# Kernel optimization log

Hardware: AMD Instinct MI355X
Metric: run time of the kernel (lower is better)

Reference implementation:

```python
import jax, jax.numpy as jnp
import numpy as np

B, HORIZON, F, ORDER, K = 8192, 64, 64, 16, 256


def setup_inputs() -> dict:
    key = jax.random.key(0)
    ks = jax.random.split(key, 7)
    s = 0.05
    x = jax.random.normal(ks[0], (B, HORIZON, F), dtype=jnp.float32)
    y0 = jax.random.normal(ks[1], (B, ORDER), dtype=jnp.float32)
    kernel = jax.random.normal(ks[2], (F + ORDER, 4 * K), dtype=jnp.float32) * s
    rec_kernel = jax.random.normal(ks[3], (K, 4 * K), dtype=jnp.float32) * s
    bias = jax.random.normal(ks[4], (4 * K,), dtype=jnp.float32) * s
    dense_w = jax.random.normal(ks[5], (K, 1), dtype=jnp.float32) * s
    dense_b = jax.random.normal(ks[6], (1,), dtype=jnp.float32) * s
    return {"x": x, "y0": y0, "kernel": kernel, "rec_kernel": rec_kernel,
            "bias": bias, "dense_w": dense_w, "dense_b": dense_b}


def reference(x, y0, kernel, rec_kernel, bias, dense_w, dense_b):
    Bn = x.shape[0]
    Ku = rec_kernel.shape[0]
    h0 = jnp.zeros((Bn, Ku), x.dtype)
    c0 = jnp.zeros((Bn, Ku), x.dtype)

    def step(carry, x_t):
        h, c, yp = carry  # yp: [B, order], newest prediction first
        inp = jnp.concatenate([x_t, yp], axis=1)          # [B, F+order]
        z = inp @ kernel + h @ rec_kernel + bias          # [B, 4K]
        i, f, g, o = jnp.split(z, 4, axis=1)              # Keras gate order i,f,c,o
        i = jax.nn.sigmoid(i)
        f = jax.nn.sigmoid(f)
        g = jnp.tanh(g)
        o = jax.nn.sigmoid(o)
        c_new = f * c + i * g
        h_new = o * jnp.tanh(c_new)
        pred = h_new @ dense_w + dense_b                  # [B, 1]
        # tf.roll(shift=1)[:, 1:] then concat([pred, .]) == shift-in newest pred
        yp_new = jnp.concatenate([pred, yp[:, :-1]], axis=1)
        return (h_new, c_new, yp_new), pred

    xs = jnp.transpose(x, (1, 0, 2))                      # [horizon, B, F]
    _, preds = jax.lax.scan(step, (h0, c0, y0), xs)       # preds: [horizon, B, 1]
    return jnp.transpose(preds, (1, 0, 2))                # [B, horizon, 1]
```

## Files before the change

### kernel.cpp

```cpp
#include <hip/hip_runtime.h>
#include <stdint.h>


typedef short v8s __attribute__((ext_vector_type(8)));
typedef float v4f __attribute__((ext_vector_type(4)));

#define NKS 11
#define NKCOL 1024
#define PKR 1
#define PKL 2
#define SK0 (PKR + PKL)

__device__ __forceinline__ unsigned bf16u(float f) {
  unsigned u = __float_as_uint(f);
  return (u + 0x7FFFu + ((u >> 16) & 1u)) >> 16;
}
__device__ __forceinline__ float sigm(float x) {
  return __builtin_amdgcn_rcpf(1.f + __expf(-x));
}
__device__ __forceinline__ float tanh_(float x) {
  return 1.f - 2.f * __builtin_amdgcn_rcpf(1.f + __expf(2.f * x));
}
__device__ __forceinline__ int a_addr(int m, int k) {
  return (((m >> 4) * NKS + (k >> 5)) << 10)
       + ((((k >> 3) & 3) * 16 + (m & 15)) << 4)
       + ((k & 7) << 1);
}

__global__ void prep_w(const float* __restrict__ ker, const float* __restrict__ rec,
                       uint4* __restrict__ wsw) {
  int tid = blockIdx.x * 256 + threadIdx.x;
  int lane = tid & 63;
  int rest = tid >> 6;
  int ks = rest % NKS;
  int nt = rest / NKS;
  int n  = nt * 16 + (lane & 15);
  int k0 = ks * 32 + ((lane >> 4) & 3) * 8;
  unsigned h[8];
  #pragma unroll
  for (int j = 0; j < 8; ++j) {
    int k = k0 + j;
    float v = 0.f;
    if (k < 80)       v = ker[k * NKCOL + n];
    else if (k < 336) v = rec[(k - 80) * NKCOL + n];
    h[j] = bf16u(v);
  }
  uint4 o;
  o.x = h[0] | (h[1] << 16); o.y = h[2] | (h[3] << 16);
  o.z = h[4] | (h[5] << 16); o.w = h[6] | (h[7] << 16);
  wsw[tid] = o;
}

__global__ __launch_bounds__(512, 2)
void lstm_main(const float* __restrict__ x, const float* __restrict__ y0,
               const float* __restrict__ bias, const float* __restrict__ dw,
               const float* __restrict__ db, const v8s* __restrict__ wv,
               float* __restrict__ out) {
  __shared__ __align__(16) char a_lds[2 * NKS * 1024];
  __shared__ __align__(16) v8s w_lds[PKL * 64 * 64];
  __shared__ float predbuf[32][8];
  __shared__ float predf[32];

  const int tid  = threadIdx.x;
  const int lane = tid & 63;
  const int wave = tid >> 6;
  const int l15  = lane & 15;
  const int quad = lane >> 4;
  const int b0   = blockIdx.x * 32;

  for (int i = tid; i < 2 * NKS * 256; i += 512) ((unsigned*)a_lds)[i] = 0;
  for (int i = tid; i < PKL * 64 * 64; i += 512) {
    int ksl = i >> 12;
    int nt  = (i >> 6) & 63;
    int ln  = i & 63;
    w_lds[i] = wv[(nt * NKS + PKR + ksl) * 64 + ln];
  }

  float bias_v[8];
  int wb[8], wlo[8];
  #pragma unroll
  for (int ln = 0; ln < 8; ++ln) {
    int g = ln >> 1, s = ln & 1;
    int ntg = g * 16 + wave * 2 + s;
    wb[ln]  = ntg * NKS * 64;
    wlo[ln] = ntg * 64 + lane;
    bias_v[ln] = bias[ntg * 16 + l15];
  }
  float dw_v[2];
  dw_v[0] = dw[wave * 32 + l15];
  dw_v[1] = dw[wave * 32 + 16 + l15];
  const float dbv = db[0];

  v8s wreg[8];
  #pragma unroll
  for (int ln = 0; ln < 8; ++ln)
    wreg[ln] = wv[wb[ln] + lane];

  float cst[2][2][4];
  #pragma unroll
  for (int mt = 0; mt < 2; ++mt)
    #pragma unroll
    for (int s = 0; s < 2; ++s)
      #pragma unroll
      for (int r = 0; r < 4; ++r) cst[mt][s][r] = 0.f;

  const int ms_x  = tid >> 3;
  const int kq8_x = tid & 7;
  const int ms_y  = (tid - 256) >> 3;
  const int jj    = tid & 7;
  float4 xpa, xpb;
  if (tid < 256) {
    const float* xp = x + ((size_t)((b0 + ms_x) * 64)) * 64 + kq8_x * 8;
    xpa = ((const float4*)xp)[0];
    xpb = ((const float4*)xp)[1];
  }

  __syncthreads();

  #pragma unroll 1
  for (int t = 0; t < 64; ++t) {
    unsigned xw[4];
    unsigned short q0 = 0, q1 = 0;
    float pin = 0.f;
    if (tid < 256) {
      xw[0] = bf16u(xpa.x) | (bf16u(xpa.y) << 16);
      xw[1] = bf16u(xpa.z) | (bf16u(xpa.w) << 16);
      xw[2] = bf16u(xpb.x) | (bf16u(xpb.y) << 16);
      xw[3] = bf16u(xpb.z) | (bf16u(xpb.w) << 16);
    } else {
      if (t == 0) {
        q0 = (unsigned short)bf16u(y0[(b0 + ms_y) * 16 + 2 * jj]);
        q1 = (unsigned short)bf16u(y0[(b0 + ms_y) * 16 + 2 * jj + 1]);
      } else {
        q0 = *(const unsigned short*)(a_lds + a_addr(ms_y, 64 + 2 * jj));
        q1 = *(const unsigned short*)(a_lds + a_addr(ms_y, 64 + 2 * jj + 1));
        pin = predf[ms_y];
      }
    }
    __syncthreads();
    if (tid < 256) {
      uint4 w4; w4.x = xw[0]; w4.y = xw[1]; w4.z = xw[2]; w4.w = xw[3];
      *(uint4*)(a_lds + a_addr(ms_x, kq8_x * 8)) = w4;
    } else {
      if (t == 0) {
        *(unsigned short*)(a_lds + a_addr(ms_y, 64 + 2 * jj))     = q0;
        *(unsigned short*)(a_lds + a_addr(ms_y, 64 + 2 * jj + 1)) = q1;
      } else {
        if (jj < 7) {
          *(unsigned short*)(a_lds + a_addr(ms_y, 64 + 2 * jj + 1)) = q0;
          *(unsigned short*)(a_lds + a_addr(ms_y, 64 + 2 * jj + 2)) = q1;
        } else {
          *(unsigned short*)(a_lds + a_addr(ms_y, 79)) = q0;
        }
        if (jj == 0)
          *(unsigned short*)(a_lds + a_addr(ms_y, 64)) = (unsigned short)bf16u(pin);
      }
    }
    __syncthreads();

    if (t < 63 && tid < 256) {
      const float* xp = x + ((size_t)((b0 + ms_x) * 64 + (t + 1))) * 64 + kq8_x * 8;
      xpa = ((const float4*)xp)[0];
      xpb = ((const float4*)xp)[1];
    }

    v4f acc[2][8];
    #pragma unroll
    for (int mt = 0; mt < 2; ++mt)
      #pragma unroll
      for (int ln = 0; ln < 8; ++ln) acc[mt][ln] = v4f{0.f, 0.f, 0.f, 0.f};

    v8s bs0[8], bs1[8];
    #pragma unroll
    for (int ln = 0; ln < 8; ++ln) bs0[ln] = wv[wb[ln] + SK0 * 64 + lane];
    v8s af0 = *(const v8s*)(a_lds + (lane << 4));
    v8s af1 = *(const v8s*)(a_lds + (NKS << 10) + (lane << 4));

    #define MFMA_BLK(ksi, W8)                                                   \
      do {                                                                      \
        v8s c0 = af0, c1 = af1;                                                 \
        if ((ksi) < NKS - 1) {                                                  \
          af0 = *(const v8s*)(a_lds + (((ksi) + 1) << 10) + (lane << 4));       \
          af1 = *(const v8s*)(a_lds + ((NKS + (ksi) + 1) << 10) + (lane << 4)); \
        }                                                                       \
        _Pragma("unroll")                                                       \
        for (int ln = 0; ln < 8; ++ln) {                                        \
          acc[0][ln] = __builtin_amdgcn_mfma_f32_16x16x32_bf16(c0, W8[ln], acc[0][ln], 0, 0, 0); \
          acc[1][ln] = __builtin_amdgcn_mfma_f32_16x16x32_bf16(c1, W8[ln], acc[1][ln], 0, 0, 0); \
        }                                                                       \
      } while (0)
    #define REFILL(BUF, rks)                                                    \
      do {                                                                      \
        _Pragma("unroll")                                                       \
        for (int ln = 0; ln < 8; ++ln)                                          \
          BUF[ln] = wv[wb[ln] + (rks) * 64 + lane];                             \
      } while (0)

    MFMA_BLK(0, wreg);

    {
      v8s wl[8];
      #pragma unroll
      for (int ln = 0; ln < 8; ++ln) wl[ln] = w_lds[wlo[ln]];
      REFILL(bs1, SK0 + 1);
      MFMA_BLK(1, wl);
      #pragma unroll
      for (int ln = 0; ln < 8; ++ln) wl[ln] = w_lds[4096 + wlo[ln]];
      MFMA_BLK(2, wl);
    }

    MFMA_BLK(3, bs0);  REFILL(bs0, 5);
    MFMA_BLK(4, bs1);  REFILL(bs1, 6);
    MFMA_BLK(5, bs0);  REFILL(bs0, 7);
    MFMA_BLK(6, bs1);  REFILL(bs1, 8);
    MFMA_BLK(7, bs0);  REFILL(bs0, 9);
    MFMA_BLK(8, bs1);  REFILL(bs1, 10);
    MFMA_BLK(9, bs0);
    MFMA_BLK(10, bs1);

    #undef MFMA_BLK
    #undef REFILL

    __syncthreads();

    float padd[2][4];
    #pragma unroll
    for (int mt = 0; mt < 2; ++mt)
      #pragma unroll
      for (int r = 0; r < 4; ++r) padd[mt][r] = 0.f;

    #pragma unroll
    for (int mt = 0; mt < 2; ++mt) {
      #pragma unroll
      for (int s = 0; s < 2; ++s) {
        const int kk = 80 + wave * 32 + s * 16 + l15;
        #pragma unroll
        for (int r = 0; r < 4; ++r) {
          float zi = acc[mt][0 + s][r] + bias_v[0 + s];
          float zf = acc[mt][2 + s][r] + bias_v[2 + s];
          float zg = acc[mt][4 + s][r] + bias_v[4 + s];
          float zo = acc[mt][6 + s][r] + bias_v[6 + s];
          float is = sigm(zi), fs = sigm(zf), gs = tanh_(zg), os = sigm(zo);
          float cn = fs * cst[mt][s][r] + is * gs;
          cst[mt][s][r] = cn;
          float hh = os * tanh_(cn);
          int m = mt * 16 + quad * 4 + r;
          *(unsigned short*)(a_lds + a_addr(m, kk)) = (unsigned short)bf16u(hh);
          padd[mt][r] += hh * dw_v[s];
        }
      }
    }
    #pragma unroll
    for (int mt = 0; mt < 2; ++mt) {
      #pragma unroll
      for (int r = 0; r < 4; ++r) {
        float p = padd[mt][r];
        p += __shfl_xor(p, 1);
        p += __shfl_xor(p, 2);
        p += __shfl_xor(p, 4);
        p += __shfl_xor(p, 8);
        if (l15 == 0) predbuf[mt * 16 + quad * 4 + r][wave] = p;
      }
    }
    __syncthreads();
    if (tid < 32) {
      float p = dbv;
      #pragma unroll
      for (int w = 0; w < 8; ++w) p += predbuf[tid][w];
      out[(size_t)(b0 + tid) * 64 + t] = p;
      predf[tid] = p;
    }
    __syncthreads();
  }
}

extern "C" void kernel_launch(void* const* d_in, const int* in_sizes, int n_in,
                              void* d_out, int out_size, void* d_ws, size_t ws_size,
                              hipStream_t stream) {
  const float* x    = (const float*)d_in[0];
  const float* y0   = (const float*)d_in[1];
  const float* ker  = (const float*)d_in[2];
  const float* rec  = (const float*)d_in[3];
  const float* bias = (const float*)d_in[4];
  const float* dw   = (const float*)d_in[5];
  const float* db   = (const float*)d_in[6];

  prep_w<<<dim3(176), dim3(256), 0, stream>>>(ker, rec, (uint4*)d_ws);
  lstm_main<<<dim3(256), dim3(512), 0, stream>>>(x, y0, bias, dw, db,
                                                 (const v8s*)d_ws, (float*)d_out);
}
```

Measured before the change: 1.292 ms.

## Reorder weight staging, prefetch global weights across steps, batch output stores

Moves the first two k-slices of weights into LDS instead of one register slice plus two LDS slices. The first two global weight slices are now preloaded before the time loop and refilled at the end of each step, so the loads for the next step overlap the current step's tail. The x prefetch for the next step moves after the MFMA section, and predictions are buffered in LDS and written as float4 every 16 steps instead of as scalar stores every step. This aims to hide global load latency and cut uncoalesced stores, at the cost of holding two weight register buffers for the whole loop, which raises register pressure.

```diff
diff --git a/kernel.cpp b/kernel.cpp
--- a/kernel.cpp
+++ b/kernel.cpp
@@ -7,9 +7,8 @@
 
 #define NKS 11
 #define NKCOL 1024
-#define PKR 1
 #define PKL 2
-#define SK0 (PKR + PKL)
+#define SK0 PKL
 
 __device__ __forceinline__ unsigned bf16u(float f) {
   unsigned u = __float_as_uint(f);
@@ -59,6 +58,7 @@
   __shared__ __align__(16) char a_lds[2 * NKS * 1024];
   __shared__ __align__(16) v8s w_lds[PKL * 64 * 64];
   __shared__ float predbuf[32][8];
+  __shared__ __align__(16) float predall[32][16];
   __shared__ float predf[32];
 
   const int tid  = threadIdx.x;
@@ -73,7 +73,7 @@
     int ksl = i >> 12;
     int nt  = (i >> 6) & 63;
     int ln  = i & 63;
-    w_lds[i] = wv[(nt * NKS + PKR + ksl) * 64 + ln];
+    w_lds[i] = wv[(nt * NKS + ksl) * 64 + ln];
   }
 
   float bias_v[8];
@@ -91,11 +91,6 @@
   dw_v[1] = dw[wave * 32 + 16 + l15];
   const float dbv = db[0];
 
-  v8s wreg[8];
-  #pragma unroll
-  for (int ln = 0; ln < 8; ++ln)
-    wreg[ln] = wv[wb[ln] + lane];
-
   float cst[2][2][4];
   #pragma unroll
   for (int mt = 0; mt < 2; ++mt)
@@ -103,6 +98,17 @@
     for (int s = 0; s < 2; ++s)
       #pragma unroll
       for (int r = 0; r < 4; ++r) cst[mt][s][r] = 0.f;
+
+  #define REFILL(BUF, rks)                                                    \
+    do {                                                                      \
+      _Pragma("unroll")                                                       \
+      for (int ln = 0; ln < 8; ++ln)                                          \
+        BUF[ln] = wv[wb[ln] + (rks) * 64 + lane];                             \
+    } while (0)
+
+  v8s bs0[8], bs1[8];
+  REFILL(bs0, SK0);
+  REFILL(bs1, SK0 + 1);
 
   const int ms_x  = tid >> 3;
   const int kq8_x = tid & 7;
@@ -158,21 +164,12 @@
     }
     __syncthreads();
 
-    if (t < 63 && tid < 256) {
-      const float* xp = x + ((size_t)((b0 + ms_x) * 64 + (t + 1))) * 64 + kq8_x * 8;
-      xpa = ((const float4*)xp)[0];
-      xpb = ((const float4*)xp)[1];
-    }
-
     v4f acc[2][8];
     #pragma unroll
     for (int mt = 0; mt < 2; ++mt)
       #pragma unroll
       for (int ln = 0; ln < 8; ++ln) acc[mt][ln] = v4f{0.f, 0.f, 0.f, 0.f};
 
-    v8s bs0[8], bs1[8];
-    #pragma unroll
-    for (int ln = 0; ln < 8; ++ln) bs0[ln] = wv[wb[ln] + SK0 * 64 + lane];
     v8s af0 = *(const v8s*)(a_lds + (lane << 4));
     v8s af1 = *(const v8s*)(a_lds + (NKS << 10) + (lane << 4));
 
@@ -189,39 +186,41 @@
           acc[1][ln] = __builtin_amdgcn_mfma_f32_16x16x32_bf16(c1, W8[ln], acc[1][ln], 0, 0, 0); \
         }                                                                       \
       } while (0)
-    #define REFILL(BUF, rks)                                                    \
+    #define MFMA_BLK_LDS(ksi, OFF)                                              \
       do {                                                                      \
+        v8s c0 = af0, c1 = af1;                                                 \
+        af0 = *(const v8s*)(a_lds + (((ksi) + 1) << 10) + (lane << 4));         \
+        af1 = *(const v8s*)(a_lds + ((NKS + (ksi) + 1) << 10) + (lane << 4));   \
         _Pragma("unroll")                                                       \
-        for (int ln = 0; ln < 8; ++ln)                                          \
-          BUF[ln] = wv[wb[ln] + (rks) * 64 + lane];                             \
+        for (int ln = 0; ln < 8; ++ln) {                                        \
+          v8s w = w_lds[(OFF) + wlo[ln]];                                       \
+          acc[0][ln] = __builtin_amdgcn_mfma_f32_16x16x32_bf16(c0, w, acc[0][ln], 0, 0, 0); \
+          acc[1][ln] = __builtin_amdgcn_mfma_f32_16x16x32_bf16(c1, w, acc[1][ln], 0, 0, 0); \
+        }                                                                       \
       } while (0)
 
-    MFMA_BLK(0, wreg);
-
-    {
-      v8s wl[8];
-      #pragma unroll
-      for (int ln = 0; ln < 8; ++ln) wl[ln] = w_lds[wlo[ln]];
-      REFILL(bs1, SK0 + 1);
-      MFMA_BLK(1, wl);
-      #pragma unroll
-      for (int ln = 0; ln < 8; ++ln) wl[ln] = w_lds[4096 + wlo[ln]];
-      MFMA_BLK(2, wl);
-    }
-
-    MFMA_BLK(3, bs0);  REFILL(bs0, 5);
-    MFMA_BLK(4, bs1);  REFILL(bs1, 6);
-    MFMA_BLK(5, bs0);  REFILL(bs0, 7);
-    MFMA_BLK(6, bs1);  REFILL(bs1, 8);
-    MFMA_BLK(7, bs0);  REFILL(bs0, 9);
-    MFMA_BLK(8, bs1);  REFILL(bs1, 10);
-    MFMA_BLK(9, bs0);
-    MFMA_BLK(10, bs1);
+    MFMA_BLK_LDS(0, 0);
+    MFMA_BLK_LDS(1, 4096);
+    MFMA_BLK(2, bs0);   REFILL(bs0, 4);
+    MFMA_BLK(3, bs1);   REFILL(bs1, 5);
+    MFMA_BLK(4, bs0);   REFILL(bs0, 6);
+    MFMA_BLK(5, bs1);   REFILL(bs1, 7);
+    MFMA_BLK(6, bs0);   REFILL(bs0, 8);
+    MFMA_BLK(7, bs1);   REFILL(bs1, 9);
+    MFMA_BLK(8, bs0);   REFILL(bs0, 10);
+    MFMA_BLK(9, bs1);   REFILL(bs1, SK0 + 1);
+    MFMA_BLK(10, bs0);  REFILL(bs0, SK0);
 
     #undef MFMA_BLK
-    #undef REFILL
-
-    __syncthreads();
+    #undef MFMA_BLK_LDS
+
+    __syncthreads();
+
+    if (t < 63 && tid < 256) {
+      const float* xp = x + ((size_t)((b0 + ms_x) * 64 + (t + 1))) * 64 + kq8_x * 8;
+      xpa = ((const float4*)xp)[0];
+      xpb = ((const float4*)xp)[1];
+    }
 
     float padd[2][4];
     #pragma unroll
@@ -267,11 +266,17 @@
       float p = dbv;
       #pragma unroll
       for (int w = 0; w < 8; ++w) p += predbuf[tid][w];
-      out[(size_t)(b0 + tid) * 64 + t] = p;
+      predall[tid][t & 15] = p;
       predf[tid] = p;
     }
     __syncthreads();
-  }
+    if ((t & 15) == 15 && tid < 128) {
+      int row = tid >> 2, c4 = (tid & 3) << 2;
+      float4 v = *(const float4*)&predall[row][c4];
+      *(float4*)&out[(size_t)(b0 + row) * 64 + (t - 15) + c4] = v;
+    }
+  }
+  #undef REFILL
 }
 
 extern "C" void kernel_launch(void* const* d_in, const int* in_sizes, int n_in,
```

After: 1.505 ms. 1.16x slower.
